# Kernel optimization log

Hardware: AMD Instinct MI355X
Metric: run time of the kernel (lower is better)

The kernel has to match this reference:

```python
import jax, jax.numpy as jnp
import numpy as np

EMBED_DIM = 1024
NUM_HEADS = 8
HEAD_DIM = EMBED_DIM // NUM_HEADS  # 128; only used for the softmax scale


def setup_inputs() -> dict:
    key = jax.random.key(0)
    ks = jax.random.split(key, 7)
    B, S, D = 4, 2048, EMBED_DIM
    scale = 1.0 / np.sqrt(D)
    x = jax.random.normal(ks[0], (B, S, D), dtype=jnp.float32)
    Wq = jax.random.normal(ks[1], (D, D), dtype=jnp.float32) * scale
    Wk = jax.random.normal(ks[2], (D, D), dtype=jnp.float32) * scale
    Wv = jax.random.normal(ks[3], (D, D), dtype=jnp.float32) * scale
    bq = jnp.zeros((D,), dtype=jnp.float32)
    bk = jnp.zeros((D,), dtype=jnp.float32)
    bv = jnp.zeros((D,), dtype=jnp.float32)
    return {"x": x, "Wq": Wq, "bq": bq, "Wk": Wk, "bk": bk, "Wv": Wv, "bv": bv}


def reference(x, Wq, bq, Wk, bk, Wv, bv):
    # q/k/v projections: note the module does NOT split heads; q,k,v stay [B,S,D]
    q = jnp.einsum("bsd,de->bse", x, Wq) + bq
    k = jnp.einsum("bsd,de->bse", x, Wk) + bk
    v = jnp.einsum("bsd,de->bse", x, Wv) + bv
    # scores: [B, S, S], scaled by head_dim**-0.5 (head_dim = D // num_heads)
    scores = jnp.einsum("bqd,bkd->bqk", q, k) / jnp.sqrt(jnp.float32(HEAD_DIM))
    attn = jax.nn.softmax(scores, axis=-1)
    # dropout is identity at inference
    out = jnp.einsum("bqk,bkd->bqd", attn, v)
    return out
```

## Files before the change

kernel.cpp:

```cpp
#include <hip/hip_runtime.h>
#include <hip/hip_bf16.h>
#include <math.h>

typedef __attribute__((ext_vector_type(8))) short  short8;
typedef __attribute__((ext_vector_type(4))) short  short4v;
typedef __attribute__((ext_vector_type(4))) float  floatx4;

#define GLD16(gp, lp) __builtin_amdgcn_global_load_lds( \
    (__attribute__((address_space(1))) void*)(void*)(gp), \
    (__attribute__((address_space(3))) void*)(lp), 16, 0, 0)

template <int MODE>
__device__ __forceinline__
void gemm_core(const unsigned short* __restrict__ A,
               const unsigned short* __restrict__ Bt,
               const float* __restrict__ bias,
               void* __restrict__ Cout,
               int lda, int ldb, int ldc, int K,
               long sA, long sB, long sC,
               float scale,
               unsigned short* __restrict__ VT,
               float* __restrict__ rowsum)
{
    __shared__ __align__(16) unsigned short smem[16384];
    unsigned short* As = smem;
    unsigned short* Bs = smem + 8192;

    const int z = blockIdx.z;
    A  += (long)z * sA;
    Bt += (long)z * sB;

    int tx_, ty_;
    {
        const int GX  = gridDim.x;
        const int f   = blockIdx.y * GX + blockIdx.x;
        const int xcd = f & 7;
        const int s   = f >> 3;
        if (MODE == 1) {
            tx_ = (xcd & 1) * 12 + s % 12;
            ty_ = (xcd >> 1) * 16 + s / 12;
        } else if (MODE == 2) {
            tx_ = (xcd & 3) * 4 + (s & 3);
            ty_ = (xcd >> 2) * 8 + (s >> 2);
        } else {
            tx_ = (xcd & 1) * 4 + (s & 3);
            ty_ = (xcd >> 1) * 4 + (s >> 2);
        }
    }
    const int m0 = ty_ * 128;
    const int n0 = tx_ * 128;

    const int t   = threadIdx.x;
    const int w   = t >> 6;
    const int l15 = t & 15;
    const int lq  = (t & 63) >> 4;
    const int wm  = w >> 1;
    const int wn  = w & 1;

    long gOffA[4], gOffB[4];
    int  lOff[4];
#pragma unroll
    for (int i = 0; i < 4; ++i) {
        int cid = i * 256 + t;
        int r   = cid >> 3;
        int c   = cid & 7;
        int cg  = c ^ (r & 7);
        lOff[i]  = cid * 8;
        gOffA[i] = (long)(m0 + r) * lda + cg * 8;
        gOffB[i] = (long)(n0 + r) * ldb + cg * 8;
    }

    floatx4 acc[4][4];
#pragma unroll
    for (int i = 0; i < 4; ++i)
#pragma unroll
        for (int j = 0; j < 4; ++j)
            acc[i][j] = (floatx4){0.f, 0.f, 0.f, 0.f};

    for (int k0 = 0; k0 < K; k0 += 64) {
#pragma unroll
        for (int i = 0; i < 4; ++i) {
            GLD16(A  + gOffA[i] + k0, &As[lOff[i]]);
            GLD16(Bt + gOffB[i] + k0, &Bs[lOff[i]]);
        }
        __syncthreads();

#pragma unroll
        for (int s = 0; s < 2; ++s) {
            short8 af[4], bf[4];
#pragma unroll
            for (int mt = 0; mt < 4; ++mt) {
                int r  = wm * 64 + mt * 16 + l15;
                int cc = (s * 4 + lq) ^ (r & 7);
                af[mt] = *(const short8*)&As[r * 64 + cc * 8];
            }
#pragma unroll
            for (int nt = 0; nt < 4; ++nt) {
                int r  = wn * 64 + nt * 16 + l15;
                int cc = (s * 4 + lq) ^ (r & 7);
                bf[nt] = *(const short8*)&Bs[r * 64 + cc * 8];
            }
#pragma unroll
            for (int mt = 0; mt < 4; ++mt)
#pragma unroll
                for (int nt = 0; nt < 4; ++nt)
                    acc[mt][nt] = __builtin_amdgcn_mfma_f32_16x16x32_bf16(
                        af[mt], bf[nt], acc[mt][nt], 0, 0, 0);
        }
        __syncthreads();
    }

    if (MODE == 1) {
        if (n0 < 2048) {
#pragma unroll
            for (int nt = 0; nt < 4; ++nt) {
                int n = n0 + wn * 64 + nt * 16 + l15;
                float bb = bias[n];
#pragma unroll
                for (int mt = 0; mt < 4; ++mt) {
                    int mBase = m0 + wm * 64 + mt * 16 + lq * 4;
#pragma unroll
                    for (int r = 0; r < 4; ++r) {
                        float v = acc[mt][nt][r] + bb;
                        ((__hip_bfloat16*)Cout)[(long)(mBase + r) * ldc + n] =
                            __float2bfloat16(v);
                    }
                }
            }
        } else {
            const int  z2  = m0 >> 11;
            const int  s0l = m0 & 2047;
            const int  d0  = n0 - 2048;
            __hip_bfloat16* T = (__hip_bfloat16*)smem;
#pragma unroll
            for (int p = 0; p < 2; ++p) {
                __syncthreads();
                if (wn == p) {
#pragma unroll
                    for (int nt = 0; nt < 4; ++nt) {
                        int nl = nt * 16 + l15;
                        float bb = bias[n0 + p * 64 + nl];
#pragma unroll
                        for (int mt = 0; mt < 4; ++mt)
#pragma unroll
                            for (int r = 0; r < 4; ++r) {
                                int ml = wm * 64 + mt * 16 + lq * 4 + r;
                                T[nl * 136 + ml] =
                                    __float2bfloat16(acc[mt][nt][r] + bb);
                            }
                    }
                }
                __syncthreads();
#pragma unroll
                for (int pass = 0; pass < 4; ++pass) {
                    int row = pass * 16 + (t >> 4);
                    int mc  = (t & 15) * 8;
                    short8 val = *(const short8*)&T[row * 136 + mc];
                    *(short8*)&VT[(long)z2 * (1024L * 2048) +
                                  (long)(d0 + p * 64 + row) * 2048 + s0l + mc] = val;
                }
            }
        }
    } else if (MODE == 2) {
        float* rs = rowsum + (long)z * 2048;
#pragma unroll
        for (int mt = 0; mt < 4; ++mt) {
#pragma unroll
            for (int r = 0; r < 4; ++r) {
                int m = m0 + wm * 64 + mt * 16 + lq * 4 + r;
                float psum = 0.f;
#pragma unroll
                for (int nt = 0; nt < 4; ++nt) {
                    int n = n0 + wn * 64 + nt * 16 + l15;
                    float e = __expf(acc[mt][nt][r] * scale);
                    __hip_bfloat16 eb = __float2bfloat16(e);
                    ((__hip_bfloat16*)Cout)[(long)z * sC + (long)m * ldc + n] = eb;
                    psum += __bfloat162float(eb);
                }
                psum += __shfl_xor(psum, 1);
                psum += __shfl_xor(psum, 2);
                psum += __shfl_xor(psum, 4);
                psum += __shfl_xor(psum, 8);
                if (l15 == 0) atomicAdd(&rs[m], psum);
            }
        }
    } else {
        const float* rs = rowsum + (long)z * 2048;
#pragma unroll
        for (int mt = 0; mt < 4; ++mt) {
            int mBase = m0 + wm * 64 + mt * 16 + lq * 4;
            float inv[4];
#pragma unroll
            for (int r = 0; r < 4; ++r) inv[r] = 1.0f / rs[mBase + r];
#pragma unroll
            for (int nt = 0; nt < 4; ++nt) {
                int n = n0 + wn * 64 + nt * 16 + l15;
#pragma unroll
                for (int r = 0; r < 4; ++r)
                    ((float*)Cout)[(long)z * sC + (long)(mBase + r) * ldc + n] =
                        acc[mt][nt][r] * inv[r];
            }
        }
    }
}

__global__ __launch_bounds__(256, 2)
void qkv128(const unsigned short* __restrict__ A, const unsigned short* __restrict__ Bt,
            const float* __restrict__ bias, void* __restrict__ Cout,
            int lda, int ldb, int ldc, int K, long sA, long sB, long sC,
            float scale, unsigned short* __restrict__ VT, float* __restrict__ rowsum)
{ gemm_core<1>(A, Bt, bias, Cout, lda, ldb, ldc, K, sA, sB, sC, scale, VT, rowsum); }

__global__ __launch_bounds__(256, 2)
void score128(const unsigned short* __restrict__ A, const unsigned short* __restrict__ Bt,
              const float* __restrict__ bias, void* __restrict__ Cout,
              int lda, int ldb, int ldc, int K, long sA, long sB, long sC,
              float scale, unsigned short* __restrict__ VT, float* __restrict__ rowsum)
{ gemm_core<2>(A, Bt, bias, Cout, lda, ldb, ldc, K, sA, sB, sC, scale, VT, rowsum); }

__global__ __launch_bounds__(256, 2)
void pv128(const unsigned short* __restrict__ A, const unsigned short* __restrict__ Bt,
           const float* __restrict__ bias, void* __restrict__ Cout,
           int lda, int ldb, int ldc, int K, long sA, long sB, long sC,
           float scale, unsigned short* __restrict__ VT, float* __restrict__ rowsum)
{ gemm_core<3>(A, Bt, bias, Cout, lda, ldb, ldc, K, sA, sB, sC, scale, VT, rowsum); }

__global__ __launch_bounds__(256)
void prep(const float* __restrict__ x,
          const float* __restrict__ Wq, const float* __restrict__ Wk,
          const float* __restrict__ Wv,
          const float* __restrict__ bq, const float* __restrict__ bk,
          const float* __restrict__ bv,
          __hip_bfloat16* __restrict__ xbf,
          __hip_bfloat16* __restrict__ WT3,
          float* __restrict__ bc,
          float* __restrict__ rs)
{
    __shared__ float tile[32][33];
    const int b = blockIdx.x;
    const int t = threadIdx.x;

    if (b < 8192) {
        long i = ((long)b * 256 + t) * 4;
        float4 v = *(const float4*)(x + i);
        union { short4v s; __hip_bfloat16 h[4]; } u;
        u.h[0] = __float2bfloat16(v.x);
        u.h[1] = __float2bfloat16(v.y);
        u.h[2] = __float2bfloat16(v.z);
        u.h[3] = __float2bfloat16(v.w);
        *(short4v*)(xbf + i) = u.s;
    } else if (b < 8192 + 3072) {
        const int idx = b - 8192;
        const int zz  = idx >> 10;
        const int rem = idx & 1023;
        const float* src = (zz == 0) ? Wq : (zz == 1) ? Wk : Wv;
        __hip_bfloat16* dst = WT3 + (long)zz * 1048576;
        const int c0 = (rem & 31) * 32, r0 = (rem >> 5) * 32;
        const int tx = t & 31, ty = t >> 5;
#pragma unroll
        for (int i = 0; i < 4; ++i)
            tile[ty + 8 * i][tx] = src[(long)(r0 + ty + 8 * i) * 1024 + c0 + tx];
        __syncthreads();
#pragma unroll
        for (int i = 0; i < 4; ++i)
            dst[(long)(c0 + ty + 8 * i) * 1024 + r0 + tx] =
                __float2bfloat16(tile[tx][ty + 8 * i]);
    } else if (b < 8192 + 3072 + 12) {
        int i = (b - (8192 + 3072)) * 256 + t;
        bc[i] = (i < 1024) ? bq[i] : (i < 2048) ? bk[i - 1024] : bv[i - 2048];
    } else {
#pragma unroll
        for (int i = 0; i < 32; ++i)
            rs[t + 256 * i] = 0.f;
    }
}

extern "C" void kernel_launch(void* const* d_in, const int* in_sizes, int n_in,
                              void* d_out, int out_size, void* d_ws, size_t ws_size,
                              hipStream_t stream)
{
    const float* x  = (const float*)d_in[0];
    const float* Wq = (const float*)d_in[1];
    const float* bq = (const float*)d_in[2];
    const float* Wk = (const float*)d_in[3];
    const float* bk = (const float*)d_in[4];
    const float* Wv = (const float*)d_in[5];
    const float* bv = (const float*)d_in[6];

    char* ws = (char*)d_ws;
    const long MB = 1048576;
    __hip_bfloat16* QKV = (__hip_bfloat16*)(ws);
    unsigned short* VT  = (unsigned short*)(ws + 48 * MB);
    __hip_bfloat16* WT3 = (__hip_bfloat16*)(ws + 64 * MB);
    float*          bc  = (float*)         (ws + 70 * MB);
    float*          rs  = (float*)         (ws + 70 * MB + 16384);
    __hip_bfloat16* xbf = (__hip_bfloat16*)(ws + 72 * MB);
    __hip_bfloat16* Pu  = (__hip_bfloat16*)(ws + 72 * MB);

    prep<<<8192 + 3072 + 12 + 1, 256, 0, stream>>>(
        x, Wq, Wk, Wv, bq, bk, bv, xbf, WT3, bc, rs);

    qkv128<<<dim3(24, 64, 1), 256, 0, stream>>>(
        (const unsigned short*)xbf, (const unsigned short*)WT3, bc, QKV,
        1024, 1024, 3072, 1024, 0, 0, 0, 1.f, VT, nullptr);

    score128<<<dim3(16, 16, 4), 256, 0, stream>>>(
        (const unsigned short*)QKV, (const unsigned short*)(QKV + 1024),
        nullptr, Pu,
        3072, 3072, 2048, 1024,
        2048L * 3072, 2048L * 3072, 2048L * 2048,
        0.08838834764831845f, nullptr, rs);

    pv128<<<dim3(8, 16, 4), 256, 0, stream>>>(
        (const unsigned short*)Pu, VT, nullptr, (float*)d_out,
        2048, 2048, 1024, 2048,
        2048L * 2048, 1024L * 2048, 2048L * 1024,
        1.f, nullptr, rs);
}
```

Measured before the change: 226.2 us.

## Fuse all four stages into one persistent cooperative kernel with grid syncs

```diff
diff --git a/kernel.cpp b/kernel.cpp
--- a/kernel.cpp
+++ b/kernel.cpp
@@ -1,6 +1,9 @@
 #include <hip/hip_runtime.h>
 #include <hip/hip_bf16.h>
+#include <hip/hip_cooperative_groups.h>
 #include <math.h>
+
+namespace cg = cooperative_groups;
 
 typedef __attribute__((ext_vector_type(8))) short  short8;
 typedef __attribute__((ext_vector_type(4))) short  short4v;
@@ -10,30 +13,89 @@
     (__attribute__((address_space(1))) void*)(void*)(gp), \
     (__attribute__((address_space(3))) void*)(lp), 16, 0, 0)
 
+struct FusedArgs {
+    const float* x;
+    const float* Wq; const float* Wk; const float* Wv;
+    const float* bq; const float* bk; const float* bv;
+    __hip_bfloat16* xbf;
+    __hip_bfloat16* WT3;
+    float*          bc;
+    float*          rs;
+    __hip_bfloat16* QKV;
+    unsigned short* VT;
+    __hip_bfloat16* Pu;
+    float*          out;
+};
+
+__device__ __forceinline__
+void prep_unit(int b, int t, float* tile , const FusedArgs& P)
+{
+    if (b < 8192) {
+        long i = ((long)b * 256 + t) * 4;
+        float4 v = *(const float4*)(P.x + i);
+        union { short4v s; __hip_bfloat16 h[4]; } u;
+        u.h[0] = __float2bfloat16(v.x);
+        u.h[1] = __float2bfloat16(v.y);
+        u.h[2] = __float2bfloat16(v.z);
+        u.h[3] = __float2bfloat16(v.w);
+        *(short4v*)(P.xbf + i) = u.s;
+    } else if (b < 11264) {
+        const int idx = b - 8192;
+        const int zz  = idx >> 10;
+        const int rem = idx & 1023;
+        const float* src = (zz == 0) ? P.Wq : (zz == 1) ? P.Wk : P.Wv;
+        __hip_bfloat16* dst = P.WT3 + (long)zz * 1048576;
+        const int c0 = (rem & 31) * 32, r0 = (rem >> 5) * 32;
+        const int tx = t & 31, ty = t >> 5;
+#pragma unroll
+        for (int i = 0; i < 4; ++i)
+            tile[(ty + 8 * i) * 33 + tx] =
+                src[(long)(r0 + ty + 8 * i) * 1024 + c0 + tx];
+        __syncthreads();
+#pragma unroll
+        for (int i = 0; i < 4; ++i)
+            dst[(long)(c0 + ty + 8 * i) * 1024 + r0 + tx] =
+                __float2bfloat16(tile[tx * 33 + ty + 8 * i]);
+        __syncthreads();
+    } else if (b < 11276) {
+        int i = (b - 11264) * 256 + t;
+        P.bc[i] = (i < 1024) ? P.bq[i] : (i < 2048) ? P.bk[i - 1024] : P.bv[i - 2048];
+    } else {
+#pragma unroll
+        for (int i = 0; i < 32; ++i)
+            P.rs[t + 256 * i] = 0.f;
+    }
+}
+
 template <int MODE>
 __device__ __forceinline__
-void gemm_core(const unsigned short* __restrict__ A,
-               const unsigned short* __restrict__ Bt,
-               const float* __restrict__ bias,
-               void* __restrict__ Cout,
-               int lda, int ldb, int ldc, int K,
-               long sA, long sB, long sC,
-               float scale,
-               unsigned short* __restrict__ VT,
-               float* __restrict__ rowsum)
-{
-    __shared__ __align__(16) unsigned short smem[16384];
+void gemm_tile(unsigned short* smem , int f, int z,
+               const FusedArgs& P)
+{
+    const unsigned short* A;
+    const unsigned short* Bt;
+    int lda, ldb, ldc, K;
+    long sA, sB, sC;
+    if (MODE == 1) {
+        A = (const unsigned short*)P.xbf; Bt = (const unsigned short*)P.WT3;
+        lda = 1024; ldb = 1024; ldc = 3072; K = 1024; sA = 0; sB = 0; sC = 0;
+    } else if (MODE == 2) {
+        A = (const unsigned short*)P.QKV; Bt = (const unsigned short*)P.QKV + 1024;
+        lda = 3072; ldb = 3072; ldc = 2048; K = 1024;
+        sA = 2048L * 3072; sB = 2048L * 3072; sC = 2048L * 2048;
+    } else {
+        A = (const unsigned short*)P.Pu; Bt = P.VT;
+        lda = 2048; ldb = 2048; ldc = 1024; K = 2048;
+        sA = 2048L * 2048; sB = 1024L * 2048; sC = 2048L * 1024;
+    }
+    A  += (long)z * sA;
+    Bt += (long)z * sB;
+
     unsigned short* As = smem;
     unsigned short* Bs = smem + 8192;
 
-    const int z = blockIdx.z;
-    A  += (long)z * sA;
-    Bt += (long)z * sB;
-
     int tx_, ty_;
     {
-        const int GX  = gridDim.x;
-        const int f   = blockIdx.y * GX + blockIdx.x;
         const int xcd = f & 7;
         const int s   = f >> 3;
         if (MODE == 1) {
@@ -115,15 +177,14 @@
 #pragma unroll
             for (int nt = 0; nt < 4; ++nt) {
                 int n = n0 + wn * 64 + nt * 16 + l15;
-                float bb = bias[n];
+                float bb = P.bc[n];
 #pragma unroll
                 for (int mt = 0; mt < 4; ++mt) {
                     int mBase = m0 + wm * 64 + mt * 16 + lq * 4;
 #pragma unroll
                     for (int r = 0; r < 4; ++r) {
                         float v = acc[mt][nt][r] + bb;
-                        ((__hip_bfloat16*)Cout)[(long)(mBase + r) * ldc + n] =
-                            __float2bfloat16(v);
+                        P.QKV[(long)(mBase + r) * ldc + n] = __float2bfloat16(v);
                     }
                 }
             }
@@ -139,7 +200,7 @@
 #pragma unroll
                     for (int nt = 0; nt < 4; ++nt) {
                         int nl = nt * 16 + l15;
-                        float bb = bias[n0 + p * 64 + nl];
+                        float bb = P.bc[n0 + p * 64 + nl];
 #pragma unroll
                         for (int mt = 0; mt < 4; ++mt)
 #pragma unroll
@@ -156,13 +217,15 @@
                     int row = pass * 16 + (t >> 4);
                     int mc  = (t & 15) * 8;
                     short8 val = *(const short8*)&T[row * 136 + mc];
-                    *(short8*)&VT[(long)z2 * (1024L * 2048) +
-                                  (long)(d0 + p * 64 + row) * 2048 + s0l + mc] = val;
+                    *(short8*)&P.VT[(long)z2 * (1024L * 2048) +
+                                    (long)(d0 + p * 64 + row) * 2048 + s0l + mc] = val;
                 }
             }
+            __syncthreads();
         }
     } else if (MODE == 2) {
-        float* rs = rowsum + (long)z * 2048;
+        float* rsz = P.rs + (long)z * 2048;
+        const float scale = 0.08838834764831845f;
 #pragma unroll
         for (int mt = 0; mt < 4; ++mt) {
 #pragma unroll
@@ -174,30 +237,30 @@
                     int n = n0 + wn * 64 + nt * 16 + l15;
                     float e = __expf(acc[mt][nt][r] * scale);
                     __hip_bfloat16 eb = __float2bfloat16(e);
-                    ((__hip_bfloat16*)Cout)[(long)z * sC + (long)m * ldc + n] = eb;
+                    P.Pu[(long)z * sC + (long)m * ldc + n] = eb;
                     psum += __bfloat162float(eb);
                 }
                 psum += __shfl_xor(psum, 1);
                 psum += __shfl_xor(psum, 2);
                 psum += __shfl_xor(psum, 4);
                 psum += __shfl_xor(psum, 8);
-                if (l15 == 0) atomicAdd(&rs[m], psum);
+                if (l15 == 0) atomicAdd(&rsz[m], psum);
             }
         }
     } else {
-        const float* rs = rowsum + (long)z * 2048;
+        const float* rsz = P.rs + (long)z * 2048;
 #pragma unroll
         for (int mt = 0; mt < 4; ++mt) {
             int mBase = m0 + wm * 64 + mt * 16 + lq * 4;
             float inv[4];
 #pragma unroll
-            for (int r = 0; r < 4; ++r) inv[r] = 1.0f / rs[mBase + r];
+            for (int r = 0; r < 4; ++r) inv[r] = 1.0f / rsz[mBase + r];
 #pragma unroll
             for (int nt = 0; nt < 4; ++nt) {
                 int n = n0 + wn * 64 + nt * 16 + l15;
 #pragma unroll
                 for (int r = 0; r < 4; ++r)
-                    ((float*)Cout)[(long)z * sC + (long)(mBase + r) * ldc + n] =
+                    P.out[(long)z * sC + (long)(mBase + r) * ldc + n] =
                         acc[mt][nt][r] * inv[r];
             }
         }
@@ -205,115 +268,91 @@
 }
 
 __global__ __launch_bounds__(256, 2)
-void qkv128(const unsigned short* __restrict__ A, const unsigned short* __restrict__ Bt,
-            const float* __restrict__ bias, void* __restrict__ Cout,
-            int lda, int ldb, int ldc, int K, long sA, long sB, long sC,
-            float scale, unsigned short* __restrict__ VT, float* __restrict__ rowsum)
-{ gemm_core<1>(A, Bt, bias, Cout, lda, ldb, ldc, K, sA, sB, sC, scale, VT, rowsum); }
-
-__global__ __launch_bounds__(256, 2)
-void score128(const unsigned short* __restrict__ A, const unsigned short* __restrict__ Bt,
-              const float* __restrict__ bias, void* __restrict__ Cout,
-              int lda, int ldb, int ldc, int K, long sA, long sB, long sC,
-              float scale, unsigned short* __restrict__ VT, float* __restrict__ rowsum)
-{ gemm_core<2>(A, Bt, bias, Cout, lda, ldb, ldc, K, sA, sB, sC, scale, VT, rowsum); }
-
-__global__ __launch_bounds__(256, 2)
-void pv128(const unsigned short* __restrict__ A, const unsigned short* __restrict__ Bt,
-           const float* __restrict__ bias, void* __restrict__ Cout,
-           int lda, int ldb, int ldc, int K, long sA, long sB, long sC,
-           float scale, unsigned short* __restrict__ VT, float* __restrict__ rowsum)
-{ gemm_core<3>(A, Bt, bias, Cout, lda, ldb, ldc, K, sA, sB, sC, scale, VT, rowsum); }
-
-__global__ __launch_bounds__(256)
-void prep(const float* __restrict__ x,
-          const float* __restrict__ Wq, const float* __restrict__ Wk,
-          const float* __restrict__ Wv,
-          const float* __restrict__ bq, const float* __restrict__ bk,
-          const float* __restrict__ bv,
-          __hip_bfloat16* __restrict__ xbf,
-          __hip_bfloat16* __restrict__ WT3,
-          float* __restrict__ bc,
-          float* __restrict__ rs)
-{
-    __shared__ float tile[32][33];
+void fused(FusedArgs P)
+{
+    __shared__ __align__(16) unsigned short smem[16384];
     const int b = blockIdx.x;
     const int t = threadIdx.x;
-
-    if (b < 8192) {
-        long i = ((long)b * 256 + t) * 4;
-        float4 v = *(const float4*)(x + i);
-        union { short4v s; __hip_bfloat16 h[4]; } u;
-        u.h[0] = __float2bfloat16(v.x);
-        u.h[1] = __float2bfloat16(v.y);
-        u.h[2] = __float2bfloat16(v.z);
-        u.h[3] = __float2bfloat16(v.w);
-        *(short4v*)(xbf + i) = u.s;
-    } else if (b < 8192 + 3072) {
-        const int idx = b - 8192;
-        const int zz  = idx >> 10;
-        const int rem = idx & 1023;
-        const float* src = (zz == 0) ? Wq : (zz == 1) ? Wk : Wv;
-        __hip_bfloat16* dst = WT3 + (long)zz * 1048576;
-        const int c0 = (rem & 31) * 32, r0 = (rem >> 5) * 32;
-        const int tx = t & 31, ty = t >> 5;
-#pragma unroll
-        for (int i = 0; i < 4; ++i)
-            tile[ty + 8 * i][tx] = src[(long)(r0 + ty + 8 * i) * 1024 + c0 + tx];
-        __syncthreads();
-#pragma unroll
-        for (int i = 0; i < 4; ++i)
-            dst[(long)(c0 + ty + 8 * i) * 1024 + r0 + tx] =
-                __float2bfloat16(tile[tx][ty + 8 * i]);
-    } else if (b < 8192 + 3072 + 12) {
-        int i = (b - (8192 + 3072)) * 256 + t;
-        bc[i] = (i < 1024) ? bq[i] : (i < 2048) ? bk[i - 1024] : bv[i - 2048];
-    } else {
-#pragma unroll
-        for (int i = 0; i < 32; ++i)
-            rs[t + 256 * i] = 0.f;
-    }
+    cg::grid_group grid = cg::this_grid();
+
+    for (int u = b; u < 11277; u += 512)
+        prep_unit(u, t, (float*)smem, P);
+    __threadfence();
+    grid.sync();
+
+    for (int f0 = b; f0 < 1536; f0 += 512)
+        gemm_tile<1>(smem, f0, 0, P);
+    __threadfence();
+    grid.sync();
+
+    for (int f0 = b; f0 < 1024; f0 += 512)
+        gemm_tile<2>(smem, f0 & 255, f0 >> 8, P);
+    __threadfence();
+    grid.sync();
+
+    gemm_tile<3>(smem, b & 127, b >> 7, P);
+}
+
+__global__ __launch_bounds__(256)
+void prepK(FusedArgs P)
+{
+    __shared__ __align__(16) float tile[32 * 33];
+    prep_unit(blockIdx.x, threadIdx.x, tile, P);
+}
+
+__global__ __launch_bounds__(256, 2)
+void qkvK(FusedArgs P)
+{
+    __shared__ __align__(16) unsigned short smem[16384];
+    gemm_tile<1>(smem, blockIdx.y * gridDim.x + blockIdx.x, 0, P);
+}
+
+__global__ __launch_bounds__(256, 2)
+void scoreK(FusedArgs P)
+{
+    __shared__ __align__(16) unsigned short smem[16384];
+    gemm_tile<2>(smem, blockIdx.y * gridDim.x + blockIdx.x, blockIdx.z, P);
+}
+
+__global__ __launch_bounds__(256, 2)
+void pvK(FusedArgs P)
+{
+    __shared__ __align__(16) unsigned short smem[16384];
+    gemm_tile<3>(smem, blockIdx.y * gridDim.x + blockIdx.x, blockIdx.z, P);
 }
 
 extern "C" void kernel_launch(void* const* d_in, const int* in_sizes, int n_in,
                               void* d_out, int out_size, void* d_ws, size_t ws_size,
                               hipStream_t stream)
 {
-    const float* x  = (const float*)d_in[0];
-    const float* Wq = (const float*)d_in[1];
-    const float* bq = (const float*)d_in[2];
-    const float* Wk = (const float*)d_in[3];
-    const float* bk = (const float*)d_in[4];
-    const float* Wv = (const float*)d_in[5];
-    const float* bv = (const float*)d_in[6];
-
     char* ws = (char*)d_ws;
     const long MB = 1048576;
-    __hip_bfloat16* QKV = (__hip_bfloat16*)(ws);
-    unsigned short* VT  = (unsigned short*)(ws + 48 * MB);
-    __hip_bfloat16* WT3 = (__hip_bfloat16*)(ws + 64 * MB);
-    float*          bc  = (float*)         (ws + 70 * MB);
-    float*          rs  = (float*)         (ws + 70 * MB + 16384);
-    __hip_bfloat16* xbf = (__hip_bfloat16*)(ws + 72 * MB);
-    __hip_bfloat16* Pu  = (__hip_bfloat16*)(ws + 72 * MB);
-
-    prep<<<8192 + 3072 + 12 + 1, 256, 0, stream>>>(
-        x, Wq, Wk, Wv, bq, bk, bv, xbf, WT3, bc, rs);
-
-    qkv128<<<dim3(24, 64, 1), 256, 0, stream>>>(
-        (const unsigned short*)xbf, (const unsigned short*)WT3, bc, QKV,
-        1024, 1024, 3072, 1024, 0, 0, 0, 1.f, VT, nullptr);
-
-    score128<<<dim3(16, 16, 4), 256, 0, stream>>>(
-        (const unsigned short*)QKV, (const unsigned short*)(QKV + 1024),
-        nullptr, Pu,
-        3072, 3072, 2048, 1024,
-        2048L * 3072, 2048L * 3072, 2048L * 2048,
-        0.08838834764831845f, nullptr, rs);
-
-    pv128<<<dim3(8, 16, 4), 256, 0, stream>>>(
-        (const unsigned short*)Pu, VT, nullptr, (float*)d_out,
-        2048, 2048, 1024, 2048,
-        2048L * 2048, 1024L * 2048, 2048L * 1024,
-        1.f, nullptr, rs);
-}
+
+    FusedArgs P;
+    P.x   = (const float*)d_in[0];
+    P.Wq  = (const float*)d_in[1];
+    P.bq  = (const float*)d_in[2];
+    P.Wk  = (const float*)d_in[3];
+    P.bk  = (const float*)d_in[4];
+    P.Wv  = (const float*)d_in[5];
+    P.bv  = (const float*)d_in[6];
+    P.QKV = (__hip_bfloat16*)(ws);
+    P.VT  = (unsigned short*)(ws + 48 * MB);
+    P.WT3 = (__hip_bfloat16*)(ws + 64 * MB);
+    P.bc  = (float*)         (ws + 70 * MB);
+    P.rs  = (float*)         (ws + 70 * MB + 16384);
+    P.xbf = (__hip_bfloat16*)(ws + 72 * MB);
+    P.Pu  = (__hip_bfloat16*)(ws + 72 * MB);
+    P.out = (float*)d_out;
+
+    void* kargs[] = { (void*)&P };
+    hipError_t err = hipLaunchCooperativeKernel(
+        (const void*)fused, dim3(512, 1, 1), dim3(256, 1, 1), kargs, 0, stream);
+
+    if (err != hipSuccess) {
+        prepK<<<11277, 256, 0, stream>>>(P);
+        qkvK<<<dim3(24, 64, 1), 256, 0, stream>>>(P);
+        scoreK<<<dim3(16, 16, 4), 256, 0, stream>>>(P);
+        pvK<<<dim3(8, 16, 4), 256, 0, stream>>>(P);
+    }
+}
```

After: 604.5 us. 2.67x slower.
